# Kernel optimization log

Measured on AMD Instinct MI355X. Metric: run time of the kernel, lower is better.

Reference implementation:

```python
import jax, jax.numpy as jnp
import numpy as np

HID = 2048
NH = 16
HD = HID // NH  # 128
EPS = 1e-6
BASE = 10000.0


def _rmsnorm(x, w):
    xf = x.astype(jnp.float32)
    y = xf * jax.lax.rsqrt(jnp.mean(xf * xf, axis=-1, keepdims=True) + EPS)
    return y.astype(x.dtype) * w


def _rope_cos_sin(seq_len, dtype):
    inv_freq = 1.0 / (BASE ** (jnp.arange(0, HD, 2, dtype=jnp.float32) / HD))
    t = jnp.arange(seq_len, dtype=jnp.float32)
    freqs = jnp.outer(t, inv_freq)          # [S, HD/2]
    emb = jnp.concatenate([freqs, freqs], axis=-1)  # [S, HD]
    return jnp.cos(emb).astype(dtype), jnp.sin(emb).astype(dtype)


def _rotate_half(x):
    x1, x2 = jnp.split(x, 2, axis=-1)
    return jnp.concatenate([-x2, x1], axis=-1)


def setup_inputs() -> dict:
    key = jax.random.key(0)
    ks = jax.random.split(key, 8)
    B, S = 2, 2048
    s = 0.02
    return {
        "hidden_states": jax.random.normal(ks[0], (B, S, HID), jnp.float32),
        "Wq": jax.random.normal(ks[1], (HID, HID), jnp.float32) * s,
        "Wk": jax.random.normal(ks[2], (HID, HID), jnp.float32) * s,
        "Wv": jax.random.normal(ks[3], (HID, HID), jnp.float32) * s,
        "Wo": jax.random.normal(ks[4], (HID, HID), jnp.float32) * s,
        "w1": jax.random.normal(ks[5], (HID, HID), jnp.float32) * s,
        "w2": jax.random.normal(ks[6], (HID, HID), jnp.float32) * s,
        "w3": jax.random.normal(ks[7], (HID, HID), jnp.float32) * s,
        "ln1_w": jnp.ones((HID,), jnp.float32),
        "ln2_w": jnp.ones((HID,), jnp.float32),
    }


def reference(hidden_states, Wq, Wk, Wv, Wo, w1, w2, w3, ln1_w, ln2_w):
    B, S, _ = hidden_states.shape
    residual = hidden_states
    x = _rmsnorm(hidden_states, ln1_w)

    # projections -> [B, NH, S, HD]
    q = (x @ Wq).reshape(B, S, NH, HD).transpose(0, 2, 1, 3)
    k = (x @ Wk).reshape(B, S, NH, HD).transpose(0, 2, 1, 3)
    v = (x @ Wv).reshape(B, S, NH, HD).transpose(0, 2, 1, 3)

    cos, sin = _rope_cos_sin(S, x.dtype)  # [S, HD]
    cos = cos[None, None]  # broadcast over batch and heads
    sin = sin[None, None]
    q = q * cos + _rotate_half(q) * sin
    k = k * cos + _rotate_half(k) * sin

    scores = jnp.einsum("bhqd,bhkd->bhqk", q, k) / np.sqrt(HD).astype(np.float32)
    # no attention_mask (torch default path). fp32 softmax.
    attn = jax.nn.softmax(scores.astype(jnp.float32), axis=-1).astype(q.dtype)
    ctx = jnp.einsum("bhqk,bhkd->bhqd", attn, v)  # [B, NH, S, HD]
    ctx = ctx.transpose(0, 2, 1, 3).reshape(B, S, HID)
    attn_out = ctx @ Wo

    h = residual + attn_out
    residual = h
    y = _rmsnorm(h, ln2_w)
    mlp = (jax.nn.silu(y @ w1) * (y @ w3)) @ w2
    return residual + mlp
```

## Files before the change

kernel.cpp:

```cpp
#include <hip/hip_runtime.h>

#define HIDN 2048
#define NHEAD 16
#define HD 128
#define SEQ 2048
#define BATCH 2
#define NROWS (BATCH*SEQ)

typedef __bf16 bf16_t;
typedef bf16_t bf16x8 __attribute__((ext_vector_type(8)));
typedef float f32x4 __attribute__((ext_vector_type(4)));

#define AS1 __attribute__((address_space(1)))
#define AS3 __attribute__((address_space(3)))

__device__ __forceinline__ unsigned short f2bf(float x) {
  union { bf16_t b; unsigned short u; } cv; cv.b = (bf16_t)x; return cv.u;
}

#define MFMA16(a,b,c) __builtin_amdgcn_mfma_f32_16x16x32_bf16((a),(b),(c),0,0,0)

__device__ __forceinline__ void gload16(const void* g, void* l) {
  __builtin_amdgcn_global_load_lds((const AS1 void*)g, (AS3 void*)l, 16, 0, 0);
}

template <int TMODE>
__global__ __launch_bounds__(256) void transpose_cvt_kernel(
    const float* __restrict__ W, unsigned short* __restrict__ Wt, int half) {
  __shared__ float t[32][33];
  int bn = blockIdx.x * 32;
  int bk = blockIdx.y * 32;
  int tx = threadIdx.x & 31, ty = threadIdx.x >> 5;
#pragma unroll
  for (int i = 0; i < 4; ++i) {
    int k = bk + ty + i * 8;
    t[ty + i * 8][tx] = W[(long)k * HIDN + bn + tx];
  }
  __syncthreads();
#pragma unroll
  for (int i = 0; i < 4; ++i) {
    int n = bn + ty + i * 8;
    int dst;
    if (TMODE == 0) dst = n;
    else if (TMODE == 1) { int d = n & 127; dst = (n & ~127) | ((d & 63) << 1) | (d >> 6); }
    else dst = (n >> 4) * 32 + half * 16 + (n & 15);
    Wt[(long)dst * HIDN + bk + tx] = f2bf(t[tx][ty + i * 8]);
  }
}

__global__ void rope_table_kernel(float* __restrict__ cosT, float* __restrict__ sinT) {
  int s = blockIdx.x, d = threadIdx.x;
  float invf = powf(10000.0f, (-2.0f * (float)d) / 128.0f);
  float ang = (float)s * invf;
  cosT[s * 64 + d] = cosf(ang);
  sinT[s * 64 + d] = sinf(ang);
}

__global__ __launch_bounds__(256) void rmsnorm_kernel(
    const float* __restrict__ x, const float* __restrict__ w, unsigned short* __restrict__ out) {
  long row = blockIdx.x;
  const float* xr = x + row * HIDN;
  int c0 = threadIdx.x * 4;
  float4 v0 = *(const float4*)(xr + c0);
  float4 v1 = *(const float4*)(xr + 1024 + c0);
  float s = v0.x*v0.x + v0.y*v0.y + v0.z*v0.z + v0.w*v0.w
          + v1.x*v1.x + v1.y*v1.y + v1.z*v1.z + v1.w*v1.w;
#pragma unroll
  for (int off = 1; off < 64; off <<= 1) s += __shfl_xor(s, off);
  __shared__ float red[4];
  if ((threadIdx.x & 63) == 0) red[threadIdx.x >> 6] = s;
  __syncthreads();
  float tot = red[0] + red[1] + red[2] + red[3];
  float r = 1.0f / sqrtf(tot * (1.0f / (float)HIDN) + 1e-6f);
  float4 w0 = *(const float4*)(w + c0);
  float4 w1 = *(const float4*)(w + 1024 + c0);
  ushort4 o0, o1;
  o0.x = f2bf(v0.x * r * w0.x); o0.y = f2bf(v0.y * r * w0.y);
  o0.z = f2bf(v0.z * r * w0.z); o0.w = f2bf(v0.w * r * w0.w);
  o1.x = f2bf(v1.x * r * w1.x); o1.y = f2bf(v1.y * r * w1.y);
  o1.z = f2bf(v1.z * r * w1.z); o1.w = f2bf(v1.w * r * w1.w);
  *(ushort4*)(out + row * HIDN + c0) = o0;
  *(ushort4*)(out + row * HIDN + 1024 + c0) = o1;
}

template <int MODE>
__global__ __launch_bounds__(512, 2) void gemm256_kernel(
    const unsigned short* __restrict__ A, const unsigned short* __restrict__ Bt,
    int nbx,
    void* __restrict__ p0, void* __restrict__ p1, void* __restrict__ p2,
    const float* __restrict__ cosT, const float* __restrict__ sinT) {
  __shared__ unsigned short L[65536];
  const int tid = threadIdx.x;
  const int wave = tid >> 6, lane = tid & 63;
  const int lr = lane & 15, lkg = lane >> 4;
  const int wr = wave >> 2, wc = wave & 3;
  const int nwg = (int)gridDim.x;
  const int bid = (int)blockIdx.x;
  const int wg = (bid & 7) * (nwg >> 3) + (bid >> 3);
  const int bx = wg % nbx, by = wg / nbx;
  const long bm = (long)by * 256, bn = (long)bx * 256;
  const int srow = wave * 8 + (lane >> 3);
  const int sslot = (lane & 7) ^ (lane >> 3);
  const unsigned short* Ag = A + (bm + srow) * HIDN + sslot * 8;
  const unsigned short* Bg = Bt + (bn + srow) * HIDN + sslot * 8;
  f32x4 acc[8][4] = {};

#define STAGE256(kt2)                                                            \
  {                                                                              \
    const long ko = (long)(kt2) * 64;                                            \
    unsigned short* Ld = &L[((kt2) & 1) * 32768];                                \
    _Pragma("unroll")                                                            \
    for (int j = 0; j < 4; ++j) {                                                \
      gload16(Ag + ko + (long)j * 64 * HIDN, &Ld[(j * 64 + wave * 8) * 64]);     \
      gload16(Bg + ko + (long)j * 64 * HIDN, &Ld[16384 + (j * 64 + wave * 8) * 64]); \
    }                                                                            \
  }

  STAGE256(0);
  STAGE256(1);
  asm volatile("s_waitcnt vmcnt(8)" ::: "memory");
  __builtin_amdgcn_sched_barrier(0);
  __builtin_amdgcn_s_barrier();

  for (int kt = 0; kt < 32; ++kt) {
    const int d = kt & 1;
    const char* Lb = (const char*)L + d * 65536;
    bf16x8 bfr[4][2];
#pragma unroll
    for (int n = 0; n < 4; ++n) {
      int row = wc * 64 + n * 16 + lr;
      int x7 = row & 7;
#pragma unroll
      for (int ks = 0; ks < 2; ++ks) {
        int s = ks * 4 + lkg;
        bfr[n][ks] = *(const bf16x8*)(Lb + 32768 + row * 128 + ((s ^ x7) << 4));
      }
    }
#pragma unroll
    for (int q = 0; q < 4; ++q) {
      bf16x8 af[2][2];
#pragma unroll
      for (int mm = 0; mm < 2; ++mm) {
        int row = wr * 128 + (q * 2 + mm) * 16 + lr;
        int x7 = row & 7;
#pragma unroll
        for (int ks = 0; ks < 2; ++ks) {
          int s = ks * 4 + lkg;
          af[mm][ks] = *(const bf16x8*)(Lb + row * 128 + ((s ^ x7) << 4));
        }
      }
      __builtin_amdgcn_s_setprio(1);
#pragma unroll
      for (int mm = 0; mm < 2; ++mm)
#pragma unroll
        for (int n = 0; n < 4; ++n) {
          acc[q * 2 + mm][n] = MFMA16(af[mm][0], bfr[n][0], acc[q * 2 + mm][n]);
          acc[q * 2 + mm][n] = MFMA16(af[mm][1], bfr[n][1], acc[q * 2 + mm][n]);
        }
      __builtin_amdgcn_s_setprio(0);
    }
    if (kt == 31) break;
    asm volatile("s_waitcnt lgkmcnt(0)" ::: "memory");
    __builtin_amdgcn_sched_barrier(0);
    __builtin_amdgcn_s_barrier();
    if (kt < 30) {
      STAGE256(kt + 2);
      asm volatile("s_waitcnt vmcnt(8)" ::: "memory");
    } else {
      asm volatile("s_waitcnt vmcnt(0)" ::: "memory");
    }
    __builtin_amdgcn_sched_barrier(0);
    __builtin_amdgcn_s_barrier();
  }
#undef STAGE256

  const int gc0 = (int)bn + wc * 64;
  if (MODE == 1) {
    unsigned short* bout = (unsigned short*)p0;
#pragma unroll
    for (int m = 0; m < 8; ++m) {
      long r0 = bm + wr * 128 + m * 16 + lkg * 4;
#pragma unroll
      for (int n = 0; n < 4; n += 2) {
        int ggrp = (gc0 + n * 16) >> 5;
        long c = (long)ggrp * 16 + lr;
#pragma unroll
        for (int r = 0; r < 4; ++r) {
          float x = acc[m][n][r], g = acc[m][n + 1][r];
          float sv = x / (1.0f + __expf(-x)) * g;
          bout[(r0 + r) * 2048 + c] = f2bf(sv);
        }
      }
    }
  } else {
    int bufid = gc0 >> 11;
    unsigned short* dst = (bufid == 0) ? (unsigned short*)p0
                        : (bufid == 1) ? (unsigned short*)p1
                                       : (unsigned short*)p2;
    if (bufid == 2) {
#pragma unroll
      for (int m = 0; m < 8; ++m) {
        long r0 = bm + wr * 128 + m * 16 + lkg * 4;
#pragma unroll
        for (int n = 0; n < 4; ++n) {
          int wcol = (gc0 + n * 16 + lr) & 2047;
#pragma unroll
          for (int r = 0; r < 4; ++r) dst[(r0 + r) * 2048 + wcol] = f2bf(acc[m][n][r]);
        }
      }
    } else {
      const float qscale = (bufid == 0) ? 0.08838834764831845f : 1.0f;
#pragma unroll
      for (int m = 0; m < 8; ++m) {
        long r0 = bm + wr * 128 + m * 16 + lkg * 4;
#pragma unroll
        for (int n = 0; n < 4; ++n) {
          int wcol = (gc0 + n * 16 + lr) & 2047;
          int f = wcol & 127, hh = wcol >> 7;
          int j = f >> 1, odd = f & 1;
          int oc = hh * 128 + (odd ? 64 : 0) + j;
#pragma unroll
          for (int r = 0; r < 4; ++r) {
            long row = r0 + r;
            int s = (int)(row & (SEQ - 1));
            float cv = cosT[s * 64 + j], sn = sinT[s * 64 + j];
            float v = acc[m][n][r];
            float o = __shfl_xor(v, 1);
            float res = (odd ? (v * cv + o * sn) : (v * cv - o * sn)) * qscale;
            dst[row * 2048 + oc] = f2bf(res);
          }
        }
      }
    }
  }
}

template <int MODE>
__global__ __launch_bounds__(256) void gemm_kernel(
    const unsigned short* __restrict__ A, const unsigned short* __restrict__ Bt, int N,
    void* __restrict__ p0, const void* __restrict__ p1) {
  __shared__ unsigned short As[128 * 32];
  __shared__ unsigned short Bs[128 * 32];
  const int tid = threadIdx.x;
  const int lane = tid & 63, wave = tid >> 6;
  const int wm = (wave >> 1) * 64, wn = (wave & 1) * 64;
  const int lr = lane & 15, lkg = lane >> 4;
  const long bm = (long)blockIdx.y * 128, bn = (long)blockIdx.x * 128;
  f32x4 acc[4][4] = {};
  const int rA0 = wave * 32 + (lane >> 2);
  const int gs0 = (lane & 3) ^ ((rA0 >> 1) & 3);
  const int gs1 = (lane & 3) ^ (((rA0 + 16) >> 1) & 3);
  const unsigned short* Ag0 = A + (bm + rA0) * HIDN + gs0 * 8;
  const unsigned short* Ag1 = A + (bm + rA0 + 16) * HIDN + gs1 * 8;
  const unsigned short* Bg0 = Bt + (bn + rA0) * HIDN + gs0 * 8;
  const unsigned short* Bg1 = Bt + (bn + rA0 + 16) * HIDN + gs1 * 8;
  unsigned short* lA0 = &As[(wave * 32) * 32];
  unsigned short* lA1 = &As[(wave * 32 + 16) * 32];
  unsigned short* lB0 = &Bs[(wave * 32) * 32];
  unsigned short* lB1 = &Bs[(wave * 32 + 16) * 32];
  for (int k0 = 0; k0 < HIDN; k0 += 32) {
    __syncthreads();
    gload16(Ag0 + k0, lA0);
    gload16(Ag1 + k0, lA1);
    gload16(Bg0 + k0, lB0);
    gload16(Bg1 + k0, lB1);
    __syncthreads();
    bf16x8 af[4], bfr[4];
#pragma unroll
    for (int m = 0; m < 4; ++m) {
      int row = wm + m * 16 + lr;
      af[m] = *(const bf16x8*)((const char*)As + row * 64 + ((lkg ^ ((row >> 1) & 3)) << 4));
    }
#pragma unroll
    for (int n = 0; n < 4; ++n) {
      int row = wn + n * 16 + lr;
      bfr[n] = *(const bf16x8*)((const char*)Bs + row * 64 + ((lkg ^ ((row >> 1) & 3)) << 4));
    }
#pragma unroll
    for (int m = 0; m < 4; ++m)
#pragma unroll
      for (int n = 0; n < 4; ++n) acc[m][n] = MFMA16(af[m], bfr[n], acc[m][n]);
  }
  float* fout = (float*)p0;
  const float* addsrc = (const float*)p1;
#pragma unroll
  for (int m = 0; m < 4; ++m)
#pragma unroll
    for (int n = 0; n < 4; ++n) {
      long r0 = bm + wm + m * 16 + lkg * 4;
      long c = bn + wn + n * 16 + lr;
#pragma unroll
      for (int r = 0; r < 4; ++r) {
        long idx = (r0 + r) * 2048 + c;
        if (MODE == 2) fout[idx] = addsrc[idx] + acc[m][n][r];
        else fout[idx] = fout[idx] + acc[m][n][r];
      }
    }
}

__global__ __launch_bounds__(256) void flash_attn_kernel(
    const unsigned short* __restrict__ Q, const unsigned short* __restrict__ Kb,
    const unsigned short* __restrict__ Vb, unsigned short* __restrict__ O) {
  __shared__ unsigned short Ks[2][64 * 128];
  __shared__ unsigned short VtL[128 * 64];
  __shared__ unsigned short Ps[4][16][72];
  const int qt = blockIdx.x, h = blockIdx.y, b = blockIdx.z;
  const int tid = threadIdx.x, wave = tid >> 6, lane = tid & 63;
  const int lr = lane & 15, lkg = lane >> 4, lk = lkg * 8;
  const long rowbase = (long)b * SEQ;
  const int qrow0 = qt * 64 + wave * 16;
  bf16x8 aq[4];
#pragma unroll
  for (int ks = 0; ks < 4; ++ks)
    aq[ks] = *(const bf16x8*)(Q + (rowbase + qrow0 + lr) * HIDN + h * HD + ks * 32 + lk);
  const int kq = tid & 15, db = tid >> 4;
  const int krl = lane >> 4;
  char* vb8 = (char*)VtL;
  f32x4 acc[8] = {};
  float m_ = -3.0e38f, l_ = 0.f;
  ushort4 vreg[2][4];
#pragma unroll
  for (int j = 0; j < 4; ++j) {
    int rl = wave * 16 + j * 4 + krl;
    int slot = (lane & 15) ^ (rl & 15);
    gload16(Kb + (rowbase + rl) * HIDN + h * HD + slot * 8,
            &Ks[0][(wave * 16 + j * 4) * 128]);
  }
#pragma unroll
  for (int j = 0; j < 4; ++j)
#pragma unroll
    for (int i = 0; i < 2; ++i)
      vreg[i][j] = *(const ushort4*)(Vb + (rowbase + kq * 4 + j) * HIDN + h * HD + db * 8 + i * 4);

  for (int t = 0; t < SEQ / 64; ++t) {
    asm volatile("s_waitcnt vmcnt(0)" ::: "memory");
#pragma unroll
    for (int i = 0; i < 2; ++i)
#pragma unroll
      for (int dd = 0; dd < 4; ++dd) {
        int d = db * 8 + i * 4 + dd;
        ushort4 w;
        w.x = ((const unsigned short*)&vreg[i][0])[dd];
        w.y = ((const unsigned short*)&vreg[i][1])[dd];
        w.z = ((const unsigned short*)&vreg[i][2])[dd];
        w.w = ((const unsigned short*)&vreg[i][3])[dd];
        *(ushort4*)(vb8 + d * 128 + ((kq * 8) ^ ((d & 7) << 4))) = w;
      }
    asm volatile("s_waitcnt lgkmcnt(0)" ::: "memory");
    asm volatile("s_barrier" ::: "memory");
    if (t + 1 < SEQ / 64) {
      const long kvn = (long)(t + 1) * 64;
#pragma unroll
      for (int j = 0; j < 4; ++j) {
        int rl = wave * 16 + j * 4 + krl;
        int slot = (lane & 15) ^ (rl & 15);
        gload16(Kb + (rowbase + kvn + rl) * HIDN + h * HD + slot * 8,
                &Ks[(t + 1) & 1][(wave * 16 + j * 4) * 128]);
      }
#pragma unroll
      for (int j = 0; j < 4; ++j)
#pragma unroll
        for (int i = 0; i < 2; ++i)
          vreg[i][j] = *(const ushort4*)(Vb + (rowbase + kvn + kq * 4 + j) * HIDN + h * HD + db * 8 + i * 4);
    }
    const char* ksb = (const char*)Ks[t & 1];
    f32x4 sa[4] = {};
#pragma unroll
    for (int n = 0; n < 4; ++n) {
      int row = n * 16 + lr;
#pragma unroll
      for (int ks = 0; ks < 4; ++ks) {
        bf16x8 bk = *(const bf16x8*)(ksb + row * 256 + (((ks * 4 + lkg) ^ (row & 15)) << 4));
        sa[n] = MFMA16(bk, aq[ks], sa[n]);
      }
    }
    float pmax = sa[0][0];
#pragma unroll
    for (int n = 0; n < 4; ++n)
#pragma unroll
      for (int r = 0; r < 4; ++r) pmax = fmaxf(pmax, sa[n][r]);
    pmax = fmaxf(pmax, __shfl_xor(pmax, 16));
    pmax = fmaxf(pmax, __shfl_xor(pmax, 32));
    float mnew = fmaxf(m_, pmax);
    float corr = __expf(m_ - mnew);
    float psum = 0.f;
#pragma unroll
    for (int n = 0; n < 4; ++n)
#pragma unroll
      for (int r = 0; r < 4; ++r) {
        float p = __expf(sa[n][r] - mnew);
        sa[n][r] = p;
        psum += p;
      }
    psum += __shfl_xor(psum, 16);
    psum += __shfl_xor(psum, 32);
    l_ = l_ * corr + psum;
    m_ = mnew;
    float corr4[4];
#pragma unroll
    for (int r = 0; r < 4; ++r) corr4[r] = __shfl(corr, 4 * lkg + r);
#pragma unroll
    for (int df = 0; df < 8; ++df)
#pragma unroll
      for (int r = 0; r < 4; ++r) acc[df][r] *= corr4[r];
#pragma unroll
    for (int n = 0; n < 4; ++n) {
      ushort4 pw;
      pw.x = f2bf(sa[n][0]); pw.y = f2bf(sa[n][1]);
      pw.z = f2bf(sa[n][2]); pw.w = f2bf(sa[n][3]);
      *(ushort4*)&Ps[wave][lr][n * 16 + 4 * lkg] = pw;
    }
    bf16x8 pa0 = *(const bf16x8*)&Ps[wave][lr][lk];
    bf16x8 pa1 = *(const bf16x8*)&Ps[wave][lr][32 + lk];
#pragma unroll
    for (int df = 0; df < 8; ++df) {
      int row = df * 16 + lr;
      int sw = (row & 7) << 4;
      bf16x8 bv0 = *(const bf16x8*)(vb8 + row * 128 + ((lkg * 16) ^ sw));
      bf16x8 bv1 = *(const bf16x8*)(vb8 + row * 128 + (((4 + lkg) * 16) ^ sw));
      acc[df] = MFMA16(pa0, bv0, acc[df]);
      acc[df] = MFMA16(pa1, bv1, acc[df]);
    }
    asm volatile("s_barrier" ::: "memory");
  }
  float invl = 1.0f / l_;
  float invl4[4];
#pragma unroll
  for (int r = 0; r < 4; ++r) invl4[r] = __shfl(invl, 4 * lkg + r);
#pragma unroll
  for (int r = 0; r < 4; ++r) {
    long orow = rowbase + qrow0 + lkg * 4 + r;
#pragma unroll
    for (int df = 0; df < 8; ++df)
      O[orow * HIDN + h * HD + df * 16 + lr] = f2bf(acc[df][r] * invl4[r]);
  }
}

extern "C" void kernel_launch(void* const* d_in, const int* in_sizes, int n_in,
                              void* d_out, int out_size, void* d_ws, size_t ws_size,
                              hipStream_t stream) {
  const float* hidden = (const float*)d_in[0];
  const float* Wq = (const float*)d_in[1];
  const float* Wk = (const float*)d_in[2];
  const float* Wv = (const float*)d_in[3];
  const float* Wo = (const float*)d_in[4];
  const float* w1 = (const float*)d_in[5];
  const float* w2 = (const float*)d_in[6];
  const float* w3 = (const float*)d_in[7];
  const float* ln1 = (const float*)d_in[8];
  const float* ln2 = (const float*)d_in[9];
  float* out = (float*)d_out;

  char* ws = (char*)d_ws;
  size_t off = 0;
  auto alloc = [&](size_t bytes) -> void* {
    void* p = ws + off;
    off += (bytes + 255) & ~(size_t)255;
    return p;
  };
  unsigned short* wblk = (unsigned short*)alloc((size_t)(2048L * 6 + 2048) * HIDN * 2);
  unsigned short* wQ = wblk;
  unsigned short* wK = wblk + (size_t)2048 * HIDN;
  unsigned short* wV = wblk + (size_t)4096 * HIDN;
  unsigned short* wO = wblk + (size_t)6144 * HIDN;
  unsigned short* wG = wblk + (size_t)8192 * HIDN;
  unsigned short* wD = wblk + (size_t)12288 * HIDN;
  unsigned short* xb   = (unsigned short*)alloc((size_t)NROWS * HIDN * 2);
  unsigned short* qb   = (unsigned short*)alloc((size_t)NROWS * HIDN * 2);
  unsigned short* kb   = (unsigned short*)alloc((size_t)NROWS * HIDN * 2);
  unsigned short* vb   = (unsigned short*)alloc((size_t)NROWS * HIDN * 2);
  unsigned short* ctxb = (unsigned short*)alloc((size_t)NROWS * HIDN * 2);
  float* cosT = (float*)alloc((size_t)SEQ * 64 * 4);
  float* sinT = (float*)alloc((size_t)SEQ * 64 * 4);
  if (off > ws_size) return;

  dim3 tgrid(HIDN / 32, HIDN / 32);
  transpose_cvt_kernel<1><<<tgrid, 256, 0, stream>>>(Wq, wQ, 0);
  transpose_cvt_kernel<1><<<tgrid, 256, 0, stream>>>(Wk, wK, 0);
  transpose_cvt_kernel<0><<<tgrid, 256, 0, stream>>>(Wv, wV, 0);
  transpose_cvt_kernel<0><<<tgrid, 256, 0, stream>>>(Wo, wO, 0);
  transpose_cvt_kernel<2><<<tgrid, 256, 0, stream>>>(w1, wG, 0);
  transpose_cvt_kernel<2><<<tgrid, 256, 0, stream>>>(w3, wG, 1);
  transpose_cvt_kernel<0><<<tgrid, 256, 0, stream>>>(w2, wD, 0);
  rope_table_kernel<<<SEQ, 64, 0, stream>>>(cosT, sinT);

  rmsnorm_kernel<<<NROWS, 256, 0, stream>>>(hidden, ln1, xb);

  gemm256_kernel<0><<<(6144 / 256) * (NROWS / 256), 512, 0, stream>>>(
      xb, wQ, 6144 / 256, qb, kb, vb, cosT, sinT);

  flash_attn_kernel<<<dim3(SEQ / 64, NHEAD, BATCH), 256, 0, stream>>>(qb, kb, vb, ctxb);

  gemm_kernel<2><<<dim3(2048 / 128, NROWS / 128), 256, 0, stream>>>(
      ctxb, wO, 2048, out, hidden);

  rmsnorm_kernel<<<NROWS, 256, 0, stream>>>(out, ln2, xb);

  gemm256_kernel<1><<<(4096 / 256) * (NROWS / 256), 512, 0, stream>>>(
      xb, wG, 4096 / 256, qb, nullptr, nullptr, nullptr, nullptr);

  gemm_kernel<3><<<dim3(2048 / 128, NROWS / 128), 256, 0, stream>>>(
      qb, wD, 2048, out, nullptr);
}
```

Before: 513.0 us.

## Write V transposed from QKV GEMM, async-stage V in attention, lazy softmax rescale, merged weight transpose

The QKV GEMM epilogue now writes V in a per-head transposed [b,h,d,s] layout. This lets flash attention stage V tiles straight into double-buffered LDS with async global-to-LDS loads, replacing the register-based transpose through LDS. Online softmax skips the max update and accumulator rescale when the new tile max stays within 8 of the running max. The seven weight transpose/convert launches are merged into one kernel with 64x64 tiles and vectorized loads and stores. Risks include more LDS per block, which may lower occupancy, and the lazy rescale letting exp values grow up to e^8.

```diff
diff --git a/kernel.cpp b/kernel.cpp
--- a/kernel.cpp
+++ b/kernel.cpp
@@ -24,27 +24,47 @@
   __builtin_amdgcn_global_load_lds((const AS1 void*)g, (AS3 void*)l, 16, 0, 0);
 }
 
-template <int TMODE>
-__global__ __launch_bounds__(256) void transpose_cvt_kernel(
-    const float* __restrict__ W, unsigned short* __restrict__ Wt, int half) {
-  __shared__ float t[32][33];
-  int bn = blockIdx.x * 32;
-  int bk = blockIdx.y * 32;
-  int tx = threadIdx.x & 31, ty = threadIdx.x >> 5;
+__global__ __launch_bounds__(256) void transpose_all_kernel(
+    const float* __restrict__ Wq, const float* __restrict__ Wk,
+    const float* __restrict__ Wv, const float* __restrict__ Wo,
+    const float* __restrict__ w1, const float* __restrict__ w3,
+    const float* __restrict__ w2, unsigned short* __restrict__ wblk) {
+  const int z = blockIdx.z;
+  const float* W; unsigned short* dstb; int tmode = 0, half = 0;
+  switch (z) {
+    case 0: W = Wq; dstb = wblk;                       tmode = 1; break;
+    case 1: W = Wk; dstb = wblk + (size_t)2048 * HIDN; tmode = 1; break;
+    case 2: W = Wv; dstb = wblk + (size_t)4096 * HIDN; break;
+    case 3: W = Wo; dstb = wblk + (size_t)6144 * HIDN; break;
+    case 4: W = w1; dstb = wblk + (size_t)8192 * HIDN; tmode = 2; half = 0; break;
+    case 5: W = w3; dstb = wblk + (size_t)8192 * HIDN; tmode = 2; half = 1; break;
+    default: W = w2; dstb = wblk + (size_t)12288 * HIDN; break;
+  }
+  __shared__ float t[64][69];
+  const int tid = threadIdx.x;
+  const int bn = blockIdx.x * 64, bk = blockIdx.y * 64;
+  const int lc = (tid & 15) * 4, lrw = tid >> 4;
 #pragma unroll
   for (int i = 0; i < 4; ++i) {
-    int k = bk + ty + i * 8;
-    t[ty + i * 8][tx] = W[(long)k * HIDN + bn + tx];
+    int k = bk + lrw + i * 16;
+    float4 v = *(const float4*)(W + (long)k * HIDN + bn + lc);
+    t[lrw + i * 16][lc] = v.x; t[lrw + i * 16][lc + 1] = v.y;
+    t[lrw + i * 16][lc + 2] = v.z; t[lrw + i * 16][lc + 3] = v.w;
   }
   __syncthreads();
-#pragma unroll
-  for (int i = 0; i < 4; ++i) {
-    int n = bn + ty + i * 8;
-    int dst;
-    if (TMODE == 0) dst = n;
-    else if (TMODE == 1) { int d = n & 127; dst = (n & ~127) | ((d & 63) << 1) | (d >> 6); }
-    else dst = (n >> 4) * 32 + half * 16 + (n & 15);
-    Wt[(long)dst * HIDN + bk + tx] = f2bf(t[tx][ty + i * 8]);
+  const int nl = tid >> 2, k0 = (tid & 3) * 16;
+  int n = bn + nl;
+  int dst;
+  if (tmode == 0) dst = n;
+  else if (tmode == 1) { int d = n & 127; dst = (n & ~127) | ((d & 63) << 1) | (d >> 6); }
+  else dst = (n >> 4) * 32 + half * 16 + (n & 15);
+  unsigned short* orow = dstb + (long)dst * HIDN + bk + k0;
+#pragma unroll
+  for (int j = 0; j < 16; j += 4) {
+    ushort4 o;
+    o.x = f2bf(t[k0 + j][nl]);     o.y = f2bf(t[k0 + j + 1][nl]);
+    o.z = f2bf(t[k0 + j + 2][nl]); o.w = f2bf(t[k0 + j + 3][nl]);
+    *(ushort4*)(orow + j) = o;
   }
 }
 
@@ -194,21 +214,25 @@
     }
   } else {
     int bufid = gc0 >> 11;
-    unsigned short* dst = (bufid == 0) ? (unsigned short*)p0
-                        : (bufid == 1) ? (unsigned short*)p1
-                                       : (unsigned short*)p2;
     if (bufid == 2) {
+      unsigned short* vT = (unsigned short*)p2;
 #pragma unroll
       for (int m = 0; m < 8; ++m) {
         long r0 = bm + wr * 128 + m * 16 + lkg * 4;
+        long bq = r0 >> 11;
+        int s = (int)(r0 & 2047);
 #pragma unroll
         for (int n = 0; n < 4; ++n) {
           int wcol = (gc0 + n * 16 + lr) & 2047;
-#pragma unroll
-          for (int r = 0; r < 4; ++r) dst[(r0 + r) * 2048 + wcol] = f2bf(acc[m][n][r]);
+          int hh = wcol >> 7, dd = wcol & 127;
+          ushort4 pw;
+          pw.x = f2bf(acc[m][n][0]); pw.y = f2bf(acc[m][n][1]);
+          pw.z = f2bf(acc[m][n][2]); pw.w = f2bf(acc[m][n][3]);
+          *(ushort4*)(vT + ((bq * 16 + hh) * 128 + dd) * (long)SEQ + s) = pw;
         }
       }
     } else {
+      unsigned short* dst = (bufid == 0) ? (unsigned short*)p0 : (unsigned short*)p1;
       const float qscale = (bufid == 0) ? 0.08838834764831845f : 1.0f;
 #pragma unroll
       for (int m = 0; m < 8; ++m) {
@@ -300,9 +324,9 @@
 
 __global__ __launch_bounds__(256) void flash_attn_kernel(
     const unsigned short* __restrict__ Q, const unsigned short* __restrict__ Kb,
-    const unsigned short* __restrict__ Vb, unsigned short* __restrict__ O) {
+    const unsigned short* __restrict__ vT, unsigned short* __restrict__ O) {
   __shared__ unsigned short Ks[2][64 * 128];
-  __shared__ unsigned short VtL[128 * 64];
+  __shared__ unsigned short Vs[2][128 * 64];
   __shared__ unsigned short Ps[4][16][72];
   const int qt = blockIdx.x, h = blockIdx.y, b = blockIdx.z;
   const int tid = threadIdx.x, wave = tid >> 6, lane = tid & 63;
@@ -313,56 +337,36 @@
 #pragma unroll
   for (int ks = 0; ks < 4; ++ks)
     aq[ks] = *(const bf16x8*)(Q + (rowbase + qrow0 + lr) * HIDN + h * HD + ks * 32 + lk);
-  const int kq = tid & 15, db = tid >> 4;
+  const unsigned short* vbase = vT + ((long)(b * 16 + h) * 128) * SEQ;
   const int krl = lane >> 4;
-  char* vb8 = (char*)VtL;
+  const int vrl = lane >> 3, vch = lane & 7;
   f32x4 acc[8] = {};
   float m_ = -3.0e38f, l_ = 0.f;
-  ushort4 vreg[2][4];
-#pragma unroll
-  for (int j = 0; j < 4; ++j) {
-    int rl = wave * 16 + j * 4 + krl;
-    int slot = (lane & 15) ^ (rl & 15);
-    gload16(Kb + (rowbase + rl) * HIDN + h * HD + slot * 8,
-            &Ks[0][(wave * 16 + j * 4) * 128]);
-  }
-#pragma unroll
-  for (int j = 0; j < 4; ++j)
-#pragma unroll
-    for (int i = 0; i < 2; ++i)
-      vreg[i][j] = *(const ushort4*)(Vb + (rowbase + kq * 4 + j) * HIDN + h * HD + db * 8 + i * 4);
+
+#define STAGEKV(t_, kv0_)                                                          \
+  {                                                                                \
+    _Pragma("unroll")                                                              \
+    for (int j = 0; j < 4; ++j) {                                                  \
+      int rl = wave * 16 + j * 4 + krl;                                            \
+      int slot = (lane & 15) ^ (rl & 15);                                          \
+      gload16(Kb + (rowbase + (kv0_) + rl) * HIDN + h * HD + slot * 8,             \
+              &Ks[(t_) & 1][(wave * 16 + j * 4) * 128]);                           \
+    }                                                                              \
+    _Pragma("unroll")                                                              \
+    for (int j = 0; j < 4; ++j) {                                                  \
+      int dd = wave * 32 + j * 8 + vrl;                                            \
+      int slot = vch ^ (dd & 7);                                                   \
+      gload16(vbase + (long)dd * SEQ + (kv0_) + slot * 8,                          \
+              &Vs[(t_) & 1][(wave * 32 + j * 8) * 64]);                            \
+    }                                                                              \
+  }
+
+  STAGEKV(0, 0);
 
   for (int t = 0; t < SEQ / 64; ++t) {
     asm volatile("s_waitcnt vmcnt(0)" ::: "memory");
-#pragma unroll
-    for (int i = 0; i < 2; ++i)
-#pragma unroll
-      for (int dd = 0; dd < 4; ++dd) {
-        int d = db * 8 + i * 4 + dd;
-        ushort4 w;
-        w.x = ((const unsigned short*)&vreg[i][0])[dd];
-        w.y = ((const unsigned short*)&vreg[i][1])[dd];
-        w.z = ((const unsigned short*)&vreg[i][2])[dd];
-        w.w = ((const unsigned short*)&vreg[i][3])[dd];
-        *(ushort4*)(vb8 + d * 128 + ((kq * 8) ^ ((d & 7) << 4))) = w;
-      }
-    asm volatile("s_waitcnt lgkmcnt(0)" ::: "memory");
     asm volatile("s_barrier" ::: "memory");
-    if (t + 1 < SEQ / 64) {
-      const long kvn = (long)(t + 1) * 64;
-#pragma unroll
-      for (int j = 0; j < 4; ++j) {
-        int rl = wave * 16 + j * 4 + krl;
-        int slot = (lane & 15) ^ (rl & 15);
-        gload16(Kb + (rowbase + kvn + rl) * HIDN + h * HD + slot * 8,
-                &Ks[(t + 1) & 1][(wave * 16 + j * 4) * 128]);
-      }
-#pragma unroll
-      for (int j = 0; j < 4; ++j)
-#pragma unroll
-        for (int i = 0; i < 2; ++i)
-          vreg[i][j] = *(const ushort4*)(Vb + (rowbase + kvn + kq * 4 + j) * HIDN + h * HD + db * 8 + i * 4);
-    }
+    if (t + 1 < SEQ / 64) STAGEKV(t + 1, (long)(t + 1) * 64);
     const char* ksb = (const char*)Ks[t & 1];
     f32x4 sa[4] = {};
 #pragma unroll
@@ -381,28 +385,43 @@
       for (int r = 0; r < 4; ++r) pmax = fmaxf(pmax, sa[n][r]);
     pmax = fmaxf(pmax, __shfl_xor(pmax, 16));
     pmax = fmaxf(pmax, __shfl_xor(pmax, 32));
-    float mnew = fmaxf(m_, pmax);
-    float corr = __expf(m_ - mnew);
-    float psum = 0.f;
-#pragma unroll
-    for (int n = 0; n < 4; ++n)
-#pragma unroll
-      for (int r = 0; r < 4; ++r) {
-        float p = __expf(sa[n][r] - mnew);
-        sa[n][r] = p;
-        psum += p;
-      }
-    psum += __shfl_xor(psum, 16);
-    psum += __shfl_xor(psum, 32);
-    l_ = l_ * corr + psum;
-    m_ = mnew;
-    float corr4[4];
-#pragma unroll
-    for (int r = 0; r < 4; ++r) corr4[r] = __shfl(corr, 4 * lkg + r);
-#pragma unroll
-    for (int df = 0; df < 8; ++df)
-#pragma unroll
-      for (int r = 0; r < 4; ++r) acc[df][r] *= corr4[r];
+    if (__all(pmax - m_ <= 8.0f)) {
+      float psum = 0.f;
+#pragma unroll
+      for (int n = 0; n < 4; ++n)
+#pragma unroll
+        for (int r = 0; r < 4; ++r) {
+          float p = __expf(sa[n][r] - m_);
+          sa[n][r] = p;
+          psum += p;
+        }
+      psum += __shfl_xor(psum, 16);
+      psum += __shfl_xor(psum, 32);
+      l_ += psum;
+    } else {
+      float mnew = fmaxf(m_, pmax);
+      float corr = __expf(m_ - mnew);
+      float psum = 0.f;
+#pragma unroll
+      for (int n = 0; n < 4; ++n)
+#pragma unroll
+        for (int r = 0; r < 4; ++r) {
+          float p = __expf(sa[n][r] - mnew);
+          sa[n][r] = p;
+          psum += p;
+        }
+      psum += __shfl_xor(psum, 16);
+      psum += __shfl_xor(psum, 32);
+      l_ = l_ * corr + psum;
+      m_ = mnew;
+      float corr4[4];
+#pragma unroll
+      for (int r = 0; r < 4; ++r) corr4[r] = __shfl(corr, 4 * lkg + r);
+#pragma unroll
+      for (int df = 0; df < 8; ++df)
+#pragma unroll
+        for (int r = 0; r < 4; ++r) acc[df][r] *= corr4[r];
+    }
 #pragma unroll
     for (int n = 0; n < 4; ++n) {
       ushort4 pw;
@@ -412,17 +431,19 @@
     }
     bf16x8 pa0 = *(const bf16x8*)&Ps[wave][lr][lk];
     bf16x8 pa1 = *(const bf16x8*)&Ps[wave][lr][32 + lk];
+    const char* vsb = (const char*)Vs[t & 1];
 #pragma unroll
     for (int df = 0; df < 8; ++df) {
       int row = df * 16 + lr;
-      int sw = (row & 7) << 4;
-      bf16x8 bv0 = *(const bf16x8*)(vb8 + row * 128 + ((lkg * 16) ^ sw));
-      bf16x8 bv1 = *(const bf16x8*)(vb8 + row * 128 + (((4 + lkg) * 16) ^ sw));
+      int x7 = row & 7;
+      bf16x8 bv0 = *(const bf16x8*)(vsb + row * 128 + ((lkg ^ x7) << 4));
+      bf16x8 bv1 = *(const bf16x8*)(vsb + row * 128 + (((4 + lkg) ^ x7) << 4));
       acc[df] = MFMA16(pa0, bv0, acc[df]);
       acc[df] = MFMA16(pa1, bv1, acc[df]);
     }
     asm volatile("s_barrier" ::: "memory");
   }
+#undef STAGEKV
   float invl = 1.0f / l_;
   float invl4[4];
 #pragma unroll
@@ -460,36 +481,28 @@
   };
   unsigned short* wblk = (unsigned short*)alloc((size_t)(2048L * 6 + 2048) * HIDN * 2);
   unsigned short* wQ = wblk;
-  unsigned short* wK = wblk + (size_t)2048 * HIDN;
-  unsigned short* wV = wblk + (size_t)4096 * HIDN;
+  unsigned short* wG = wblk + (size_t)8192 * HIDN;
   unsigned short* wO = wblk + (size_t)6144 * HIDN;
-  unsigned short* wG = wblk + (size_t)8192 * HIDN;
   unsigned short* wD = wblk + (size_t)12288 * HIDN;
   unsigned short* xb   = (unsigned short*)alloc((size_t)NROWS * HIDN * 2);
   unsigned short* qb   = (unsigned short*)alloc((size_t)NROWS * HIDN * 2);
   unsigned short* kb   = (unsigned short*)alloc((size_t)NROWS * HIDN * 2);
-  unsigned short* vb   = (unsigned short*)alloc((size_t)NROWS * HIDN * 2);
+  unsigned short* vTb  = (unsigned short*)alloc((size_t)NROWS * HIDN * 2);
   unsigned short* ctxb = (unsigned short*)alloc((size_t)NROWS * HIDN * 2);
   float* cosT = (float*)alloc((size_t)SEQ * 64 * 4);
   float* sinT = (float*)alloc((size_t)SEQ * 64 * 4);
   if (off > ws_size) return;
 
-  dim3 tgrid(HIDN / 32, HIDN / 32);
-  transpose_cvt_kernel<1><<<tgrid, 256, 0, stream>>>(Wq, wQ, 0);
-  transpose_cvt_kernel<1><<<tgrid, 256, 0, stream>>>(Wk, wK, 0);
-  transpose_cvt_kernel<0><<<tgrid, 256, 0, stream>>>(Wv, wV, 0);
-  transpose_cvt_kernel<0><<<tgrid, 256, 0, stream>>>(Wo, wO, 0);
-  transpose_cvt_kernel<2><<<tgrid, 256, 0, stream>>>(w1, wG, 0);
-  transpose_cvt_kernel<2><<<tgrid, 256, 0, stream>>>(w3, wG, 1);
-  transpose_cvt_kernel<0><<<tgrid, 256, 0, stream>>>(w2, wD, 0);
+  transpose_all_kernel<<<dim3(HIDN / 64, HIDN / 64, 7), 256, 0, stream>>>(
+      Wq, Wk, Wv, Wo, w1, w3, w2, wblk);
   rope_table_kernel<<<SEQ, 64, 0, stream>>>(cosT, sinT);
 
   rmsnorm_kernel<<<NROWS, 256, 0, stream>>>(hidden, ln1, xb);
 
   gemm256_kernel<0><<<(6144 / 256) * (NROWS / 256), 512, 0, stream>>>(
-      xb, wQ, 6144 / 256, qb, kb, vb, cosT, sinT);
-
-  flash_attn_kernel<<<dim3(SEQ / 64, NHEAD, BATCH), 256, 0, stream>>>(qb, kb, vb, ctxb);
+      xb, wQ, 6144 / 256, qb, kb, vTb, cosT, sinT);
+
+  flash_attn_kernel<<<dim3(SEQ / 64, NHEAD, BATCH), 256, 0, stream>>>(qb, kb, vTb, ctxb);
 
   gemm_kernel<2><<<dim3(2048 / 128, NROWS / 128), 256, 0, stream>>>(
       ctxb, wO, 2048, out, hidden);
```

Result: faster. 477.1 us (-7.0%).
